# Performance work log

Measured on AMD Instinct MI355X. Metric: run time of the kernel, lower is better.

## Reference

```python
import jax, jax.numpy as jnp
import numpy as np

B, T, I = 256, 512, 1024
H, O = 1024, 1024


def setup_inputs() -> dict:
    key = jax.random.key(0)
    ks = jax.random.split(key, 8)
    std = 1.0 / np.sqrt(H)
    u = lambda k, shape: jax.random.uniform(k, shape, jnp.float32, -std, std)
    return {
        "x": jax.random.normal(ks[0], (B, T, I), jnp.float32),
        "Wx": u(ks[1], (4 * H, I)),   # x2h weight
        "bx": u(ks[2], (4 * H,)),     # x2h bias
        "Wh": u(ks[3], (4 * H, H)),   # h2h weight
        "bh": u(ks[4], (4 * H,)),     # h2h bias
        "c2c": u(ks[5], (3 * H,)),    # peephole weights (ci, cf, co)
        "Wfc": u(ks[6], (O, H)),      # final fc weight
        "bfc": u(ks[7], (O,)),        # final fc bias
    }


def reference(x, Wx, bx, Wh, bh, c2c, Wfc, bfc):
    Bv, Tv, _ = x.shape
    Hv = Wh.shape[1]
    # Precompute input projections for all timesteps in one GEMM: [B, T, 4H]
    xg = jnp.einsum('bti,gi->btg', x, Wx) + bx + bh
    ci, cf, co = jnp.split(c2c, 3)

    def step(carry, xg_t):
        h, c = carry                      # [B, H] each
        gates = xg_t + h @ Wh.T           # [B, 4H]
        i, f, g, o = jnp.split(gates, 4, axis=-1)
        i = jax.nn.sigmoid(i + ci * c)    # peephole into input gate
        f = jax.nn.sigmoid(f + cf * c)    # peephole into forget gate
        c_new = f * c + i * jnp.tanh(g)
        o = jax.nn.sigmoid(o + co * c_new)  # peephole into output gate
        h_new = o * jnp.tanh(c_new)
        return (h_new, c_new), None

    h0 = jnp.zeros((Bv, Hv), x.dtype)
    c0 = jnp.zeros((Bv, Hv), x.dtype)
    (hT, _), _ = jax.lax.scan(step, (h0, c0), jnp.swapaxes(xg, 0, 1))
    return hT @ Wfc.T + bfc  # [B, O]
```

## Files before the change

kernel.cpp:

```cpp
#include <hip/hip_runtime.h>
#include <hip/hip_bf16.h>

typedef __attribute__((ext_vector_type(8))) short short8;
typedef __attribute__((ext_vector_type(4))) float f32x4;

#define T_STEPS 512
#define BATCH   256
#define HDIM    1024
#define GDIM    4096

__device__ __forceinline__ float sigmoidf_(float x) {
  return 1.0f / (1.0f + __expf(-x));
}
__device__ __forceinline__ float tanh_(float x) {
  return 2.0f / (1.0f + __expf(-2.0f * x)) - 1.0f;
}
__device__ __forceinline__ short f2bf(float f) {
  __hip_bfloat16 h = __float2bfloat16(f);
  short s;
  __builtin_memcpy(&s, &h, sizeof(short));
  return s;
}

__device__ __forceinline__ void gld_lds16(const __hip_bfloat16* g, void* l) {
  __builtin_amdgcn_global_load_lds(
      (const __attribute__((address_space(1))) void*)(const void*)g,
      (__attribute__((address_space(3))) void*)l, 16, 0, 0);
}

__global__ void pack_kernel(const float* __restrict__ Wh,
                            const float* __restrict__ bx, const float* __restrict__ bh,
                            __hip_bfloat16* __restrict__ Whb,
                            float* __restrict__ biasc)
{
  const int stride = gridDim.x * blockDim.x;
  const int tid0 = blockIdx.x * blockDim.x + threadIdx.x;
  for (int i = tid0; i < GDIM * HDIM; i += stride)
    Whb[i] = __float2bfloat16(Wh[i]);
  for (int i = tid0; i < GDIM; i += stride)
    biasc[i] = bx[i] + bh[i];
}

__global__ __launch_bounds__(512, 2)
void xg_gemm(const float* __restrict__ x, const float* __restrict__ Wx,
             __hip_bfloat16* __restrict__ xg, int t0)
{
  __shared__ short8 As[2][1024];
  __shared__ short8 Bs[2][1024];

  const int tid  = threadIdx.x;
  const int wave = tid >> 6;
  const int lane = tid & 63;

  const int cpx = gridDim.x >> 3;
  const int nb  = (blockIdx.x & 7) * cpx + (blockIdx.x >> 3);
  const int nt  = nb & 31;
  const int mt  = nb >> 5;

  const int trel  = mt >> 1;
  const int brow0 = (mt & 1) * 128;

  const int r0 = tid >> 3;
  const int cg = tid & 7;

  const float* asrc0 = x + ((size_t)(brow0 + r0) * T_STEPS + (t0 + trel)) * 1024 + cg * 8;
  const float* asrc1 = x + ((size_t)(brow0 + r0 + 64) * T_STEPS + (t0 + trel)) * 1024 + cg * 8;
  const float* bsrc0 = Wx + (size_t)(nt * 128 + r0) * 1024 + cg * 8;
  const float* bsrc1 = Wx + (size_t)(nt * 128 + r0 + 64) * 1024 + cg * 8;

  const int aslot0 = r0 * 8 + (cg ^ (r0 & 7));
  const int aslot1 = (r0 + 64) * 8 + (cg ^ (r0 & 7));

  f32x4 a0l, a0h, a1l, a1h, b0l, b0h, b1l, b1h;

#define XG_LOAD(KC)                                        \
  do {                                                     \
    a0l = *(const f32x4*)(asrc0 + (KC) * 64);              \
    a0h = *(const f32x4*)(asrc0 + (KC) * 64 + 4);          \
    a1l = *(const f32x4*)(asrc1 + (KC) * 64);              \
    a1h = *(const f32x4*)(asrc1 + (KC) * 64 + 4);          \
    b0l = *(const f32x4*)(bsrc0 + (KC) * 64);              \
    b0h = *(const f32x4*)(bsrc0 + (KC) * 64 + 4);          \
    b1l = *(const f32x4*)(bsrc1 + (KC) * 64);              \
    b1h = *(const f32x4*)(bsrc1 + (KC) * 64 + 4);          \
  } while (0)

#define XG_CVT1(lo, hi, dstarr, slot)                      \
  do {                                                     \
    short8 s_;                                             \
    _Pragma("unroll")                                      \
    for (int e = 0; e < 4; ++e) {                          \
      s_[e]     = f2bf((lo)[e]);                           \
      s_[e + 4] = f2bf((hi)[e]);                           \
    }                                                      \
    dstarr[slot] = s_;                                     \
  } while (0)

#define XG_WRITE(BUF)                                      \
  do {                                                     \
    XG_CVT1(a0l, a0h, As[BUF], aslot0);                    \
    XG_CVT1(a1l, a1h, As[BUF], aslot1);                    \
    XG_CVT1(b0l, b0h, Bs[BUF], aslot0);                    \
    XG_CVT1(b1l, b1h, Bs[BUF], aslot1);                    \
  } while (0)

  const int wr = wave >> 2;
  const int wc = wave & 3;

  f32x4 acc[4][2];
#pragma unroll
  for (int m = 0; m < 4; ++m)
#pragma unroll
    for (int n = 0; n < 2; ++n) acc[m][n] = (f32x4){0.f, 0.f, 0.f, 0.f};

  XG_LOAD(0);
  XG_WRITE(0);
  __syncthreads();

#pragma unroll 1
  for (int kc = 0; kc < 16; ++kc) {
    if (kc < 15) XG_LOAD(kc + 1);
    const int bs = kc & 1;
#pragma unroll
    for (int ks = 0; ks < 2; ++ks) {
      const int cgf = ks * 4 + (lane >> 4);
      short8 af[4], bfr[2];
#pragma unroll
      for (int m = 0; m < 4; ++m) {
        const int row = wr * 64 + m * 16 + (lane & 15);
        af[m] = As[bs][row * 8 + (cgf ^ (row & 7))];
      }
#pragma unroll
      for (int n = 0; n < 2; ++n) {
        const int row = wc * 32 + n * 16 + (lane & 15);
        bfr[n] = Bs[bs][row * 8 + (cgf ^ (row & 7))];
      }
#pragma unroll
      for (int m = 0; m < 4; ++m)
#pragma unroll
        for (int n = 0; n < 2; ++n)
          acc[m][n] = __builtin_amdgcn_mfma_f32_16x16x32_bf16(af[m], bfr[n], acc[m][n], 0, 0, 0);
    }
    if (kc < 15) XG_WRITE((kc + 1) & 1);
    __syncthreads();
  }

  const int dcol = lane & 15;
  const int dr0  = (lane >> 4) * 4;
#pragma unroll
  for (int m = 0; m < 4; ++m) {
#pragma unroll
    for (int n = 0; n < 2; ++n) {
      const int ocol = nt * 128 + wc * 32 + n * 16 + dcol;
#pragma unroll
      for (int rr = 0; rr < 4; ++rr) {
        const int orow = mt * 128 + wr * 64 + m * 16 + dr0 + rr;
        xg[(size_t)orow * GDIM + ocol] = __float2bfloat16(acc[m][n][rr]);
      }
    }
  }
#undef XG_LOAD
#undef XG_CVT1
#undef XG_WRITE
}

__global__ __launch_bounds__(512, 4)
void lstm_step(const __hip_bfloat16* __restrict__ xg_t,
               const __hip_bfloat16* __restrict__ Whb,
               const float* __restrict__ biasc,
               const float* __restrict__ c2c,
               const __hip_bfloat16* __restrict__ h_in,
               __hip_bfloat16* __restrict__ h_out,
               float* __restrict__ c_st)
{
  __shared__ short8 As[2][512];
  __shared__ short8 Bs[2][512];

  const int tid  = threadIdx.x;
  const int wave = tid >> 6;
  const int lane = tid & 63;
  const int l15  = lane & 15;
  const int lg   = lane >> 4;

  const int bid   = blockIdx.x;
  const int xcd   = bid & 7;
  const int idx   = bid >> 3;
  const int ntile = xcd * 8 + (idx & 7);
  const int mtile = idx >> 3;
  const int b0 = mtile * 64;
  const int j0 = ntile * 16;

  const int srow = tid >> 3;
  const int scg  = tid & 7;
  const int sswz = scg ^ (srow & 7);
  const __hip_bfloat16* asrc = h_in + (size_t)(b0 + srow) * HDIM + sswz * 8;
  const int bgrow = (srow >> 4) * HDIM + j0 + (srow & 15);
  const __hip_bfloat16* bsrc = Whb + (size_t)bgrow * HDIM + sswz * 8;

  void* la0 = (void*)&As[0][wave * 64];
  void* la1 = (void*)&As[1][wave * 64];
  void* lb0 = (void*)&Bs[0][wave * 64];
  void* lb1 = (void*)&Bs[1][wave * 64];

  const int rf = wave & 3;
  const int kh = wave >> 2;
  const int arow = rf * 16 + l15;
  const int colg = kh * 4 + lg;
  const int aidx = arow * 8 + (colg ^ (arow & 7));
  int bidx[4];
#pragma unroll
  for (int f = 0; f < 4; ++f) {
    const int br = f * 16 + l15;
    bidx[f] = br * 8 + (colg ^ (br & 7));
  }

  f32x4 acc[4];
#pragma unroll
  for (int f = 0; f < 4; ++f) acc[f] = (f32x4){0.f, 0.f, 0.f, 0.f};

  gld_lds16(asrc, la0);
  gld_lds16(bsrc, lb0);
  __syncthreads();

#pragma unroll
  for (int kc = 0; kc < 16; ++kc) {
    if (kc < 15) {
      gld_lds16(asrc + (kc + 1) * 64, (kc & 1) ? la0 : la1);
      gld_lds16(bsrc + (kc + 1) * 64, (kc & 1) ? lb0 : lb1);
    }
    const short8* Ab = As[kc & 1];
    const short8* Bb = Bs[kc & 1];
    short8 af = Ab[aidx];
    acc[0] = __builtin_amdgcn_mfma_f32_16x16x32_bf16(af, Bb[bidx[0]], acc[0], 0, 0, 0);
    acc[1] = __builtin_amdgcn_mfma_f32_16x16x32_bf16(af, Bb[bidx[1]], acc[1], 0, 0, 0);
    acc[2] = __builtin_amdgcn_mfma_f32_16x16x32_bf16(af, Bb[bidx[2]], acc[2], 0, 0, 0);
    acc[3] = __builtin_amdgcn_mfma_f32_16x16x32_bf16(af, Bb[bidx[3]], acc[3], 0, 0, 0);
    __syncthreads();
  }

  float* red = (float*)&As[0][0];
  const int drow = lg * 4;
  const int dcol = l15;
  if (kh == 1) {
#pragma unroll
    for (int f = 0; f < 4; ++f)
#pragma unroll
      for (int r = 0; r < 4; ++r)
        red[(rf * 16 + drow + r) * 64 + f * 16 + dcol] = acc[f][r];
  }
  __syncthreads();
  if (kh == 0) {
#pragma unroll
    for (int f = 0; f < 4; ++f)
#pragma unroll
      for (int r = 0; r < 4; ++r)
        acc[f][r] += red[(rf * 16 + drow + r) * 64 + f * 16 + dcol];

    const int j = j0 + dcol;
    const float bi = biasc[j];
    const float bf = biasc[HDIM + j];
    const float bg = biasc[2 * HDIM + j];
    const float bo = biasc[3 * HDIM + j];
    const float ci = c2c[j];
    const float cf = c2c[HDIM + j];
    const float co = c2c[2 * HDIM + j];
#pragma unroll
    for (int r = 0; r < 4; ++r) {
      const int b = b0 + rf * 16 + drow + r;
      const __hip_bfloat16* xr = xg_t + (size_t)b * GDIM + j;
      float x0 = __bfloat162float(xr[0]);
      float x1 = __bfloat162float(xr[HDIM]);
      float x2 = __bfloat162float(xr[2 * HDIM]);
      float x3 = __bfloat162float(xr[3 * HDIM]);
      float cp = c_st[(size_t)b * HDIM + j];
      float ig = sigmoidf_(acc[0][r] + x0 + bi + ci * cp);
      float fg = sigmoidf_(acc[1][r] + x1 + bf + cf * cp);
      float gg = tanh_(acc[2][r] + x2 + bg);
      float cn = fg * cp + ig * gg;
      float og = sigmoidf_(acc[3][r] + x3 + bo + co * cn);
      float hn = og * tanh_(cn);
      c_st[(size_t)b * HDIM + j] = cn;
      h_out[(size_t)b * HDIM + j] = __float2bfloat16(hn);
    }
  }
}

__global__ __launch_bounds__(256, 1)
void fc_kernel(const __hip_bfloat16* __restrict__ h,
               const float* __restrict__ Wfc,
               const float* __restrict__ bfc,
               float* __restrict__ out)
{
  __shared__ short8 As8[512];
  __shared__ short8 Bs8[512];

  const int tid = threadIdx.x;
  const int wave = tid >> 6;
  const int lane = tid & 63;
  const int mtile = blockIdx.x >> 4;
  const int otile = blockIdx.x & 15;
  const int b0 = mtile * 64, o0 = otile * 64;

  const int r0 = tid >> 3;
  const int cg0 = tid & 7;

  f32x4 acc[4];
#pragma unroll
  for (int f = 0; f < 4; ++f) acc[f] = (f32x4){0.f, 0.f, 0.f, 0.f};

#pragma unroll 1
  for (int kc = 0; kc < 16; ++kc) {
    __syncthreads();
    As8[r0 * 8 + (cg0 ^ (r0 & 7))] =
        *(const short8*)(const void*)(h + (size_t)(b0 + r0) * HDIM + kc * 64 + cg0 * 8);
    As8[(r0 + 32) * 8 + (cg0 ^ (r0 & 7))] =
        *(const short8*)(const void*)(h + (size_t)(b0 + r0 + 32) * HDIM + kc * 64 + cg0 * 8);
    {
      const float* p0 = Wfc + (size_t)(o0 + r0) * HDIM + kc * 64 + cg0 * 8;
      const float* p1 = Wfc + (size_t)(o0 + r0 + 32) * HDIM + kc * 64 + cg0 * 8;
      f32x4 l0 = *(const f32x4*)p0, h0 = *(const f32x4*)(p0 + 4);
      f32x4 l1 = *(const f32x4*)p1, h1 = *(const f32x4*)(p1 + 4);
      short8 s0, s1;
#pragma unroll
      for (int e = 0; e < 4; ++e) {
        s0[e] = f2bf(l0[e]); s0[e + 4] = f2bf(h0[e]);
        s1[e] = f2bf(l1[e]); s1[e + 4] = f2bf(h1[e]);
      }
      Bs8[r0 * 8 + (cg0 ^ (r0 & 7))] = s0;
      Bs8[(r0 + 32) * 8 + (cg0 ^ (r0 & 7))] = s1;
    }
    __syncthreads();
#pragma unroll
    for (int s = 0; s < 2; ++s) {
      const int colg = s * 4 + (lane >> 4);
      const int ar = wave * 16 + (lane & 15);
      short8 af = As8[ar * 8 + (colg ^ (ar & 7))];
#pragma unroll
      for (int f = 0; f < 4; ++f) {
        const int br = f * 16 + (lane & 15);
        short8 bfq = Bs8[br * 8 + (colg ^ (br & 7))];
        acc[f] = __builtin_amdgcn_mfma_f32_16x16x32_bf16(af, bfq, acc[f], 0, 0, 0);
      }
    }
  }

  const int dcol = lane & 15;
  const int drow = (lane >> 4) * 4;
#pragma unroll
  for (int f = 0; f < 4; ++f) {
    const int o = o0 + f * 16 + dcol;
    const float bias = bfc[o];
#pragma unroll
    for (int r = 0; r < 4; ++r) {
      const int b = b0 + wave * 16 + drow + r;
      out[(size_t)b * 1024 + o] = acc[f][r] + bias;
    }
  }
}

extern "C" void kernel_launch(void* const* d_in, const int* in_sizes, int n_in,
                              void* d_out, int out_size, void* d_ws, size_t ws_size,
                              hipStream_t stream)
{
  const float* x   = (const float*)d_in[0];
  const float* Wx  = (const float*)d_in[1];
  const float* bx  = (const float*)d_in[2];
  const float* Wh  = (const float*)d_in[3];
  const float* bh  = (const float*)d_in[4];
  const float* c2c = (const float*)d_in[5];
  const float* Wfc = (const float*)d_in[6];
  const float* bfc = (const float*)d_in[7];
  float* out = (float*)d_out;

  char* ws = (char*)d_ws;
  __hip_bfloat16* Whb   = (__hip_bfloat16*)(ws);
  float*          biasc = (float*)(ws + (8u << 20));
  __hip_bfloat16* hb0   = (__hip_bfloat16*)(ws + (8u << 20) + (1u << 16));
  __hip_bfloat16* hb1   = (__hip_bfloat16*)(ws + (8u << 20) + (1u << 16) + (1u << 19));
  float*          c_st  = (float*)(ws + (8u << 20) + (1u << 16) + (1u << 20));
  __hip_bfloat16* xgbuf = (__hip_bfloat16*)(ws + (11u << 20));

  const size_t xg_off = (size_t)11 << 20;
  int W = 4;
  for (int cand = 512; cand >= 4; cand >>= 1) {
    size_t need = xg_off + (size_t)cand * BATCH * GDIM * sizeof(__hip_bfloat16);
    if (need <= ws_size) { W = cand; break; }
  }

  hipMemsetAsync(hb0, 0, (size_t)BATCH * HDIM * sizeof(__hip_bfloat16), stream);
  hipMemsetAsync(c_st, 0, (size_t)BATCH * HDIM * sizeof(float), stream);

  pack_kernel<<<1024, 256, 0, stream>>>(Wh, bx, bh, Whb, biasc);

  const int NW = T_STEPS / W;
  for (int w = 0; w < NW; ++w) {
    xg_gemm<<<W * 64, 512, 0, stream>>>(x, Wx, xgbuf, w * W);
    for (int tt = 0; tt < W; ++tt) {
      const int t = w * W + tt;
      const __hip_bfloat16* hin = (t & 1) ? hb1 : hb0;
      __hip_bfloat16* hout      = (t & 1) ? hb0 : hb1;
      lstm_step<<<256, 512, 0, stream>>>(xgbuf + (size_t)tt * BATCH * GDIM,
                                         Whb, biasc, c2c, hin, hout, c_st);
    }
  }

  fc_kernel<<<64, 256, 0, stream>>>(hb0, Wfc, bfc, out);
}
```

Baseline: 9.412 ms.

## Restructure LSTM step: weights in registers, full h tile staged in LDS

After: 8.273 ms. -12.1%, faster.

```diff
diff --git a/kernel.cpp b/kernel.cpp
--- a/kernel.cpp
+++ b/kernel.cpp
@@ -1,5 +1,6 @@
 #include <hip/hip_runtime.h>
 #include <hip/hip_bf16.h>
+#include <stdint.h>
 
 typedef __attribute__((ext_vector_type(8))) short short8;
 typedef __attribute__((ext_vector_type(4))) float f32x4;
@@ -21,6 +22,17 @@
   __builtin_memcpy(&s, &h, sizeof(short));
   return s;
 }
+__device__ __forceinline__ float bf2f(unsigned u16) {
+  unsigned u = u16 << 16;
+  float f;
+  __builtin_memcpy(&f, &u, 4);
+  return f;
+}
+
+#define AL16(dst, off, base)                                        \
+  asm volatile("global_load_dwordx4 %0, %1, %2"                     \
+               : "=v"(dst) : "v"(off), "s"(base) : "memory")
+#define VMDRAIN() asm volatile("s_waitcnt vmcnt(0)" ::: "memory")
 
 __device__ __forceinline__ void gld_lds16(const __hip_bfloat16* g, void* l) {
   __builtin_amdgcn_global_load_lds(
@@ -41,7 +53,7 @@
     biasc[i] = bx[i] + bh[i];
 }
 
-__global__ __launch_bounds__(512, 2)
+__global__ __launch_bounds__(512, 1)
 void xg_gemm(const float* __restrict__ x, const float* __restrict__ Wx,
              __hip_bfloat16* __restrict__ xg, int t0)
 {
@@ -164,7 +176,7 @@
 #undef XG_WRITE
 }
 
-__global__ __launch_bounds__(512, 4)
+__global__ __launch_bounds__(512, 1)
 void lstm_step(const __hip_bfloat16* __restrict__ xg_t,
                const __hip_bfloat16* __restrict__ Whb,
                const float* __restrict__ biasc,
@@ -173,8 +185,7 @@
                __hip_bfloat16* __restrict__ h_out,
                float* __restrict__ c_st)
 {
-  __shared__ short8 As[2][512];
-  __shared__ short8 Bs[2][512];
+  __shared__ short8 hstage[8192];
 
   const int tid  = threadIdx.x;
   const int wave = tid >> 6;
@@ -190,98 +201,99 @@
   const int b0 = mtile * 64;
   const int j0 = ntile * 16;
 
-  const int srow = tid >> 3;
-  const int scg  = tid & 7;
-  const int sswz = scg ^ (srow & 7);
-  const __hip_bfloat16* asrc = h_in + (size_t)(b0 + srow) * HDIM + sswz * 8;
-  const int bgrow = (srow >> 4) * HDIM + j0 + (srow & 15);
-  const __hip_bfloat16* bsrc = Whb + (size_t)bgrow * HDIM + sswz * 8;
-
-  void* la0 = (void*)&As[0][wave * 64];
-  void* la1 = (void*)&As[1][wave * 64];
-  void* lb0 = (void*)&Bs[0][wave * 64];
-  void* lb1 = (void*)&Bs[1][wave * 64];
-
-  const int rf = wave & 3;
-  const int kh = wave >> 2;
-  const int arow = rf * 16 + l15;
-  const int colg = kh * 4 + lg;
-  const int aidx = arow * 8 + (colg ^ (arow & 7));
-  int bidx[4];
-#pragma unroll
-  for (int f = 0; f < 4; ++f) {
-    const int br = f * 16 + l15;
-    bidx[f] = br * 8 + (colg ^ (br & 7));
-  }
+  const int gate = wave >> 1;
+  const int kh   = wave & 1;
+
+  short8 bw[16];
+  {
+    const uint64_t base = (uint64_t)Whb;
+    const unsigned off0 =
+        (unsigned)((((gate * 1024 + j0 + l15) * 1024) + kh * 512 + lg * 8) * 2);
+#pragma unroll
+    for (int c = 0; c < 16; ++c)
+      AL16(bw[c], off0 + (unsigned)(c * 64), base);
+  }
+
+#pragma unroll
+  for (int k = 0; k < 16; ++k) {
+    const int gidx = tid + k * 512;
+    const int row  = gidx >> 7;
+    const int gc   = gidx & 127;
+    gld_lds16(h_in + (size_t)(b0 + row) * HDIM + (gc ^ (row & 7)) * 8,
+              (void*)&hstage[k * 512 + wave * 64]);
+  }
+  VMDRAIN();
+  __builtin_amdgcn_sched_barrier(0);
+  __syncthreads();
 
   f32x4 acc[4];
 #pragma unroll
-  for (int f = 0; f < 4; ++f) acc[f] = (f32x4){0.f, 0.f, 0.f, 0.f};
-
-  gld_lds16(asrc, la0);
-  gld_lds16(bsrc, lb0);
+  for (int m = 0; m < 4; ++m) acc[m] = (f32x4){0.f, 0.f, 0.f, 0.f};
+
+#pragma unroll
+  for (int c = 0; c < 16; ++c) {
+    const int colg = kh * 64 + c * 4 + lg;
+#pragma unroll
+    for (int m = 0; m < 4; ++m) {
+      const int row = m * 16 + l15;
+      short8 af = hstage[row * 128 + (colg ^ (row & 7))];
+      acc[m] = __builtin_amdgcn_mfma_f32_16x16x32_bf16(af, bw[c], acc[m], 0, 0, 0);
+    }
+  }
   __syncthreads();
 
-#pragma unroll
-  for (int kc = 0; kc < 16; ++kc) {
-    if (kc < 15) {
-      gld_lds16(asrc + (kc + 1) * 64, (kc & 1) ? la0 : la1);
-      gld_lds16(bsrc + (kc + 1) * 64, (kc & 1) ? lb0 : lb1);
-    }
-    const short8* Ab = As[kc & 1];
-    const short8* Bb = Bs[kc & 1];
-    short8 af = Ab[aidx];
-    acc[0] = __builtin_amdgcn_mfma_f32_16x16x32_bf16(af, Bb[bidx[0]], acc[0], 0, 0, 0);
-    acc[1] = __builtin_amdgcn_mfma_f32_16x16x32_bf16(af, Bb[bidx[1]], acc[1], 0, 0, 0);
-    acc[2] = __builtin_amdgcn_mfma_f32_16x16x32_bf16(af, Bb[bidx[2]], acc[2], 0, 0, 0);
-    acc[3] = __builtin_amdgcn_mfma_f32_16x16x32_bf16(af, Bb[bidx[3]], acc[3], 0, 0, 0);
-    __syncthreads();
-  }
-
-  float* red = (float*)&As[0][0];
-  const int drow = lg * 4;
-  const int dcol = l15;
-  if (kh == 1) {
-#pragma unroll
-    for (int f = 0; f < 4; ++f)
+  float* redA = (float*)&hstage[0];
+  float* redB = redA + 4608;
+  {
+    float* myred = kh ? redB : redA;
+#pragma unroll
+    for (int m = 0; m < 4; ++m)
 #pragma unroll
       for (int r = 0; r < 4; ++r)
-        red[(rf * 16 + drow + r) * 64 + f * 16 + dcol] = acc[f][r];
+        myred[gate * 1152 + (m * 16 + lg * 4 + r) * 18 + l15] = acc[m][r];
   }
   __syncthreads();
-  if (kh == 0) {
-#pragma unroll
-    for (int f = 0; f < 4; ++f)
-#pragma unroll
-      for (int r = 0; r < 4; ++r)
-        acc[f][r] += red[(rf * 16 + drow + r) * 64 + f * 16 + dcol];
-
-    const int j = j0 + dcol;
-    const float bi = biasc[j];
-    const float bf = biasc[HDIM + j];
-    const float bg = biasc[2 * HDIM + j];
-    const float bo = biasc[3 * HDIM + j];
-    const float ci = c2c[j];
-    const float cf = c2c[HDIM + j];
-    const float co = c2c[2 * HDIM + j];
-#pragma unroll
-    for (int r = 0; r < 4; ++r) {
-      const int b = b0 + rf * 16 + drow + r;
-      const __hip_bfloat16* xr = xg_t + (size_t)b * GDIM + j;
-      float x0 = __bfloat162float(xr[0]);
-      float x1 = __bfloat162float(xr[HDIM]);
-      float x2 = __bfloat162float(xr[2 * HDIM]);
-      float x3 = __bfloat162float(xr[3 * HDIM]);
-      float cp = c_st[(size_t)b * HDIM + j];
-      float ig = sigmoidf_(acc[0][r] + x0 + bi + ci * cp);
-      float fg = sigmoidf_(acc[1][r] + x1 + bf + cf * cp);
-      float gg = tanh_(acc[2][r] + x2 + bg);
-      float cn = fg * cp + ig * gg;
-      float og = sigmoidf_(acc[3][r] + x3 + bo + co * cn);
-      float hn = og * tanh_(cn);
-      c_st[(size_t)b * HDIM + j] = cn;
-      h_out[(size_t)b * HDIM + j] = __float2bfloat16(hn);
-    }
+
+  {
+    const int row = tid >> 3;
+    const int c2  = (tid & 7) * 2;
+    const int j   = j0 + c2;
+    const int b   = b0 + row;
+
+    float g0[4], g1[4];
+#pragma unroll
+    for (int gg = 0; gg < 4; ++gg) {
+      const int o = gg * 1152 + row * 18 + c2;
+      unsigned u  = *(const unsigned*)&xg_t[(size_t)b * GDIM + gg * 1024 + j];
+      g0[gg] = redA[o]     + redB[o]     + biasc[gg * 1024 + j]     + bf2f(u & 0xffffu);
+      g1[gg] = redA[o + 1] + redB[o + 1] + biasc[gg * 1024 + j + 1] + bf2f(u >> 16);
+    }
+    const float ci0 = c2c[j],            ci1 = c2c[j + 1];
+    const float cf0 = c2c[HDIM + j],     cf1 = c2c[HDIM + j + 1];
+    const float co0 = c2c[2 * HDIM + j], co1 = c2c[2 * HDIM + j + 1];
+
+    float cp0 = c_st[(size_t)b * HDIM + j];
+    float cp1 = c_st[(size_t)b * HDIM + j + 1];
+
+    float ii = sigmoidf_(g0[0] + ci0 * cp0);
+    float ff = sigmoidf_(g0[1] + cf0 * cp0);
+    float gv = tanh_(g0[2]);
+    float cn0 = ff * cp0 + ii * gv;
+    float oo = sigmoidf_(g0[3] + co0 * cn0);
+    float h0 = oo * tanh_(cn0);
+
+    ii = sigmoidf_(g1[0] + ci1 * cp1);
+    ff = sigmoidf_(g1[1] + cf1 * cp1);
+    gv = tanh_(g1[2]);
+    float cn1 = ff * cp1 + ii * gv;
+    oo = sigmoidf_(g1[3] + co1 * cn1);
+    float h1 = oo * tanh_(cn1);
+
+    c_st[(size_t)b * HDIM + j]     = cn0;
+    c_st[(size_t)b * HDIM + j + 1] = cn1;
+    unsigned pk = (unsigned)(unsigned short)f2bf(h0) |
+                  ((unsigned)(unsigned short)f2bf(h1) << 16);
+    *(unsigned*)&h_out[(size_t)b * HDIM + j] = pk;
   }
 }
 
```
